# Performance work log

Hardware: AMD Instinct MI355X
Metric: run time of the kernel (lower is better)

The kernel has to match this reference:

```python
import jax, jax.numpy as jnp
import numpy as np

D_MODEL = 1024
NUM_HEADS = 16
D_K = D_MODEL // NUM_HEADS


def setup_inputs() -> dict:
    key = jax.random.key(0)
    ks = jax.random.split(key, 11)
    B, S, D = 2, 2048, D_MODEL
    scale = 1.0 / np.sqrt(D)
    inp = {
        'q': jax.random.normal(ks[0], (B, S, D), jnp.float32),
        'k': jax.random.normal(ks[1], (B, S, D), jnp.float32),
        'v': jax.random.normal(ks[2], (B, S, D), jnp.float32),
        'wq': jax.random.normal(ks[3], (D, D), jnp.float32) * scale,
        'bq': jnp.zeros((D,), jnp.float32),
        'wk': jax.random.normal(ks[4], (D, D), jnp.float32) * scale,
        'bk': jnp.zeros((D,), jnp.float32),
        'wv': jax.random.normal(ks[5], (D, D), jnp.float32) * scale,
        'bv': jnp.zeros((D,), jnp.float32),
        'wo': jax.random.normal(ks[6], (D, D), jnp.float32) * scale,
        'bo': jnp.zeros((D,), jnp.float32),
    }
    return inp


def _split_heads(x):
    B, S, _ = x.shape
    return x.reshape(B, S, NUM_HEADS, D_K).transpose(0, 2, 1, 3)  # [B,H,S,dk]


def reference(q, k, v, wq, bq, wk, bk, wv, bv, wo, bo):
    # Linear projections (torch Linear: x @ W^T + b)
    qh = _split_heads(q @ wq.T + bq)
    kh = _split_heads(k @ wk.T + bk)
    vh = _split_heads(v @ wv.T + bv)
    scores = jnp.einsum('bhqd,bhkd->bhqk', qh, kh) / np.sqrt(D_K)
    attn = jax.nn.softmax(scores, axis=-1)  # dropout is identity in eval
    ctx = jnp.einsum('bhqk,bhkd->bhqd', attn, vh)
    B, H, S, dk = ctx.shape
    ctx = ctx.transpose(0, 2, 1, 3).reshape(B, S, H * dk)
    return ctx @ wo.T + bo
```

## Files before the change

kernel.cpp:

```cpp
#include <hip/hip_runtime.h>
#include <hip/hip_bf16.h>
#include <math.h>

#define BATCH 2
#define SEQ   2048
#define DMODEL 1024
#define NHEAD 16
#define DK    64
#define M_TOT (BATCH*SEQ)
#define KDIM  DMODEL

typedef short bf16x8 __attribute__((ext_vector_type(8)));
typedef short bf16x4 __attribute__((ext_vector_type(4)));
typedef float f32x4  __attribute__((ext_vector_type(4)));
typedef __hip_bfloat16 bf16;

#define QSCALE 0.18033688011112042f

__device__ inline void gld_lds16(const void* g, void* l) {
    __builtin_amdgcn_global_load_lds(
        (const __attribute__((address_space(1))) unsigned int*)g,
        (__attribute__((address_space(3))) unsigned int*)l, 16, 0, 0);
}

__device__ inline unsigned pack2(float a, float b) {
    union { __hip_bfloat162 h; unsigned u; } t;
    t.h = __float22bfloat162_rn(make_float2(a, b));
    return t.u;
}

__global__ __launch_bounds__(256) void conv_all(
    const float* __restrict__ q, const float* __restrict__ k, const float* __restrict__ v,
    const float* __restrict__ wq, const float* __restrict__ wk,
    const float* __restrict__ wv, const float* __restrict__ wo,
    bf16* __restrict__ qh, bf16* __restrict__ kh, bf16* __restrict__ vh,
    bf16* __restrict__ wqh, bf16* __restrict__ wkh, bf16* __restrict__ wvh,
    bf16* __restrict__ woh)
{
    const int y = blockIdx.y;
    const int i = (blockIdx.x * 256 + threadIdx.x) * 4;
    if (y < 3) {
        const float* src = y == 0 ? q : (y == 1 ? k : v);
        bf16* dst = y == 0 ? qh : (y == 1 ? kh : vh);
        float4 t = *(const float4*)(src + i);
        uint2 o;
        o.x = pack2(t.x, t.y);
        o.y = pack2(t.z, t.w);
        *(uint2*)(dst + i) = o;
    } else {
        const int w = i >> 20;
        const int j = i & ((1 << 20) - 1);
        const float* src = w == 0 ? wq : (w == 1 ? wk : (w == 2 ? wv : wo));
        bf16* dsth = w == 0 ? wqh : (w == 1 ? wkh : (w == 2 ? wvh : woh));
        float4 t = *(const float4*)(src + j);
        uint2 oh;
        oh.x = pack2(t.x, t.y);
        oh.y = pack2(t.z, t.w);
        *(uint2*)(dsth + j) = oh;
    }
}

__device__ __forceinline__ void gemm_body(
    const bf16* __restrict__ Ah, const bf16* __restrict__ Wh,
    const float* __restrict__ bias, void* __restrict__ out,
    int layout, float scale, bf16* sA, bf16* sB, int kb, int ke,
    int row0, int col0)
{
    const int tid  = threadIdx.x;
    const int wave = tid >> 6, lane = tid & 63;
    const int ln   = lane & 15, quad = lane >> 4;
    const int wm   = wave >> 1, wn = wave & 1;

    const int srow = lane >> 2;
    const int clog = (lane & 3) ^ (srow & 3);
    const size_t gA0 = (size_t)(row0 + wave * 16 + srow) * KDIM + clog * 8;
    const size_t gB0 = (size_t)(col0 + wave * 16 + srow) * KDIM + clog * 8;
    const int ldsoff = (wave * 16 + srow) * 64 + (lane & 3) * 16;

    const int swz = (quad ^ (ln & 3)) * 8;

    f32x4 acc[4][4] = {};

    for (int k0 = kb; k0 < ke; k0 += 32) {
        __syncthreads();
#pragma unroll
        for (int j = 0; j < 2; ++j) {
            const size_t go = (size_t)k0 + (size_t)j * 64 * KDIM;
            gld_lds16(Ah + gA0 + go, (char*)sA + j * 4096 + ldsoff);
            gld_lds16(Wh + gB0 + go, (char*)sB + j * 4096 + ldsoff);
        }
        __syncthreads();

        bf16x8 af[4], bfr[4];
#pragma unroll
        for (int t = 0; t < 4; ++t) {
            af[t]  = *(const bf16x8*)&sA[(wm * 64 + t * 16 + ln) * 32 + swz];
            bfr[t] = *(const bf16x8*)&sB[(wn * 64 + t * 16 + ln) * 32 + swz];
        }
#pragma unroll
        for (int mt = 0; mt < 4; ++mt)
#pragma unroll
            for (int nt = 0; nt < 4; ++nt)
                acc[mt][nt] = __builtin_amdgcn_mfma_f32_16x16x32_bf16(af[mt], bfr[nt], acc[mt][nt], 0, 0, 0);
    }

#pragma unroll
    for (int nt = 0; nt < 4; ++nt) {
        const int n = col0 + wn * 64 + nt * 16 + ln;
        const float bv = (layout == 3) ? 0.f : bias[n];
#pragma unroll
        for (int mt = 0; mt < 4; ++mt) {
            const int m0 = row0 + wm * 64 + mt * 16 + quad * 4;
            if (layout == 0 || layout == 3) {
#pragma unroll
                for (int r = 0; r < 4; ++r)
                    ((float*)out)[(size_t)(m0 + r) * DMODEL + n] = (acc[mt][nt][r] + bv) * scale;
            } else if (layout == 1) {
                const int h = n >> 6, d = n & (DK - 1);
#pragma unroll
                for (int r = 0; r < 4; ++r) {
                    const int m = m0 + r;
                    const int b = m >> 11, s = m & (SEQ - 1);
                    ((bf16*)out)[((size_t)(b * NHEAD + h) * SEQ + s) * DK + d] =
                        __float2bfloat16((acc[mt][nt][r] + bv) * scale);
                }
            } else {
                const int h = n >> 6, d = n & (DK - 1);
                const int b = m0 >> 11, s0 = m0 & (SEQ - 1);
                union { bf16x4 v; uint2 u; } o4;
                o4.u.x = pack2((acc[mt][nt][0] + bv) * scale, (acc[mt][nt][1] + bv) * scale);
                o4.u.y = pack2((acc[mt][nt][2] + bv) * scale, (acc[mt][nt][3] + bv) * scale);
                *(bf16x4*)&((bf16*)out)[((size_t)(b * NHEAD + h) * DK + d) * SEQ + s0] = o4.v;
            }
        }
    }
}

struct QKVArgs {
    const bf16* A[3];
    const bf16* W[3];
    const float* bias[3];
    bf16* out[3];
    float scale[3];
    int layout[3];
};

__global__ __launch_bounds__(256) void qkv_gemm(QKVArgs a) {
    __shared__ __align__(16) bf16 sA[128 * 32];
    __shared__ __align__(16) bf16 sB[128 * 32];
    const int lin = (blockIdx.z * gridDim.y + blockIdx.y) * gridDim.x + blockIdx.x;
    const int xcd = lin & 7;
    const int r   = lin >> 3;
    const int z   = r >> 5;
    const int t   = r & 31;
    const int mt  = xcd * 4 + (t >> 3);
    const int nt  = t & 7;
    gemm_body(a.A[z], a.W[z], a.bias[z],
              (void*)a.out[z], a.layout[z], a.scale[z], sA, sB, 0, KDIM,
              mt * 128, nt * 128);
}

__global__ __launch_bounds__(256) void gemm_o(
    const bf16* __restrict__ Ah, const bf16* __restrict__ Wh,
    float* __restrict__ p0, float* __restrict__ p1)
{
    __shared__ __align__(16) bf16 sA[128 * 32];
    __shared__ __align__(16) bf16 sB[128 * 32];
    const int lin = (blockIdx.z * gridDim.y + blockIdx.y) * gridDim.x + blockIdx.x;
    const int xcd = lin & 7;
    const int r   = lin >> 3;
    const int z   = r >> 5;
    const int t   = r & 31;
    const int mt  = xcd * 4 + (t >> 3);
    const int nt  = t & 7;
    gemm_body(Ah, Wh, nullptr, (void*)(z ? p1 : p0), 3, 1.0f,
              sA, sB, z * (KDIM / 2), (z + 1) * (KDIM / 2),
              mt * 128, nt * 128);
}

__global__ __launch_bounds__(256) void combine_o(
    const float* __restrict__ p0, const float* __restrict__ p1,
    const float* __restrict__ bias, float* __restrict__ out)
{
    const int i = (blockIdx.x * 256 + threadIdx.x) * 4;
    float4 a = *(const float4*)(p0 + i);
    float4 b = *(const float4*)(p1 + i);
    float4 c = *(const float4*)(bias + (i & (DMODEL - 1)));
    float4 o;
    o.x = a.x + b.x + c.x;
    o.y = a.y + b.y + c.y;
    o.z = a.z + b.z + c.z;
    o.w = a.w + b.w + c.w;
    *(float4*)(out + i) = o;
}

#define NKT (SEQ / 64)
__global__ __launch_bounds__(256) void flash_attn_mfma(
    const bf16* __restrict__ Q, const bf16* __restrict__ K,
    const bf16* __restrict__ Vt, bf16* __restrict__ ctxh)
{
    __shared__ __align__(16) bf16 Vts[64 * 64];

    const int tid  = threadIdx.x;
    const int wave = tid >> 6, lane = tid & 63;
    const int ln   = lane & 15, quad = lane >> 4;

    const int lin  = blockIdx.y * gridDim.x + blockIdx.x;
    const int slot = lin >> 3;
    const int bh   = (lin & 7) * 4 + (slot >> 4);
    const int qt   = slot & 15;
    const int b    = bh >> 4, h = bh & (NHEAD - 1);

    const int q0 = qt * 128 + wave * 32;
    const bf16* Qb = Q + ((size_t)bh * SEQ + q0) * DK;
    bf16x8 qf[2][2];
#pragma unroll
    for (int c = 0; c < 2; ++c)
#pragma unroll
        for (int nt = 0; nt < 2; ++nt)
            qf[c][nt] = *(const bf16x8*)(Qb + (size_t)(nt * 16 + ln) * DK + c * 32 + quad * 8);

    f32x4 of[2][4] = {};
    float lp[2] = {0.f, 0.f};

    const int sr  = tid >> 2;
    const int scb = (tid & 3) * 2;
    const int ssw = sr & 7;
    const bf16* Vg0 = Vt + ((size_t)bh * DK + sr) * SEQ;
    const bf16* Kl  = K + (size_t)bh * SEQ * DK + (size_t)ln * DK + quad * 8;

    int vaddr[4];
#pragma unroll
    for (int mt = 0; mt < 4; ++mt)
        vaddr[mt] = ln * 64 + (((2 * mt + (quad >> 1)) ^ (ln & 7)) * 8) + (quad & 1) * 4;

    bf16x8 kfA[2][4], kfB[2][4];
#pragma unroll
    for (int c = 0; c < 2; ++c)
#pragma unroll
        for (int mt = 0; mt < 4; ++mt)
            kfA[c][mt] = *(const bf16x8*)(Kl + (size_t)(mt * 16) * DK + c * 32);

    auto halfiter = [&](int ktc, bf16x8 (&kfc)[2][4], bf16x8 (&kfn)[2][4]) {
        __syncthreads();
        {
            const bf16* Vg = Vg0 + ktc * 64;
            uint4 v0 = *(const uint4*)(Vg + scb * 8);
            uint4 v1 = *(const uint4*)(Vg + scb * 8 + 8);
            *(uint4*)(&Vts[sr * 64 + ((scb    ) ^ ssw) * 8]) = v0;
            *(uint4*)(&Vts[sr * 64 + ((scb + 1) ^ ssw) * 8]) = v1;
        }
        __syncthreads();

        const int ktn = (ktc + 1) & (NKT - 1);
#pragma unroll
        for (int c = 0; c < 2; ++c)
#pragma unroll
            for (int mt = 0; mt < 4; ++mt)
                kfn[c][mt] = *(const bf16x8*)(Kl + (size_t)(ktn * 64 + mt * 16) * DK + c * 32);

        f32x4 st[4][2] = {};
#pragma unroll
        for (int c = 0; c < 2; ++c)
#pragma unroll
            for (int mt = 0; mt < 4; ++mt)
#pragma unroll
                for (int nt = 0; nt < 2; ++nt)
                    st[mt][nt] = __builtin_amdgcn_mfma_f32_16x16x32_bf16(kfc[c][mt], qf[c][nt], st[mt][nt], 0, 0, 0);

        bf16x4 aP[4][2];
#pragma unroll
        for (int mt = 0; mt < 4; ++mt)
#pragma unroll
            for (int nt = 0; nt < 2; ++nt) {
                float p0 = __builtin_amdgcn_exp2f(st[mt][nt][0]);
                float p1 = __builtin_amdgcn_exp2f(st[mt][nt][1]);
                float p2 = __builtin_amdgcn_exp2f(st[mt][nt][2]);
                float p3 = __builtin_amdgcn_exp2f(st[mt][nt][3]);
                lp[nt] += (p0 + p1) + (p2 + p3);
                union { bf16x4 v; uint2 u; } uu;
                uu.u.x = pack2(p0, p1);
                uu.u.y = pack2(p2, p3);
                aP[mt][nt] = uu.v;
            }

#pragma unroll
        for (int mt = 0; mt < 4; ++mt)
#pragma unroll
            for (int nt = 0; nt < 4; ++nt) {
                bf16x4 vf = *(const bf16x4*)(&Vts[vaddr[mt] + nt * 1024]);
                of[0][nt] = __builtin_amdgcn_mfma_f32_16x16x16bf16_1k(aP[mt][0], vf, of[0][nt], 0, 0, 0);
                of[1][nt] = __builtin_amdgcn_mfma_f32_16x16x16bf16_1k(aP[mt][1], vf, of[1][nt], 0, 0, 0);
            }
    };

    for (int kt = 0; kt < NKT; kt += 2) {
        halfiter(kt,     kfA, kfB);
        halfiter(kt + 1, kfB, kfA);
    }

#pragma unroll
    for (int nt = 0; nt < 2; ++nt) {
        lp[nt] += __shfl_xor(lp[nt], 16, 64);
        lp[nt] += __shfl_xor(lp[nt], 32, 64);
    }
    float linv[2][4];
#pragma unroll
    for (int mtP = 0; mtP < 2; ++mtP)
#pragma unroll
        for (int r = 0; r < 4; ++r)
            linv[mtP][r] = 1.0f / __shfl(lp[mtP], quad * 4 + r, 64);

    const size_t base = ((size_t)b * SEQ + q0) * DMODEL + h * DK;
#pragma unroll
    for (int mtP = 0; mtP < 2; ++mtP)
#pragma unroll
        for (int nt = 0; nt < 4; ++nt)
#pragma unroll
            for (int r = 0; r < 4; ++r) {
                const float v = of[mtP][nt][r] * linv[mtP][r];
                const size_t idx = base + (size_t)(mtP * 16 + quad * 4 + r) * DMODEL + nt * 16 + ln;
                ctxh[idx] = __float2bfloat16(v);
            }
}

extern "C" void kernel_launch(void* const* d_in, const int* in_sizes, int n_in,
                              void* d_out, int out_size, void* d_ws, size_t ws_size,
                              hipStream_t stream) {
    const float* q  = (const float*)d_in[0];
    const float* k  = (const float*)d_in[1];
    const float* v  = (const float*)d_in[2];
    const float* wq = (const float*)d_in[3];
    const float* bq = (const float*)d_in[4];
    const float* wk = (const float*)d_in[5];
    const float* bk = (const float*)d_in[6];
    const float* wv = (const float*)d_in[7];
    const float* bv = (const float*)d_in[8];
    const float* wo = (const float*)d_in[9];
    const float* bo = (const float*)d_in[10];
    float* out = (float*)d_out;

    char* ws = (char*)d_ws;
    const size_t MB = 1u << 20;
    bf16* wq_hi = (bf16*)(ws + 0 * MB);
    bf16* wk_hi = (bf16*)(ws + 2 * MB);
    bf16* wv_hi = (bf16*)(ws + 4 * MB);
    bf16* wo_hi = (bf16*)(ws + 6 * MB);
    bf16* q_hi  = (bf16*)(ws + 8 * MB);
    bf16* k_hi  = (bf16*)(ws + 16 * MB);
    bf16* v_hi  = (bf16*)(ws + 24 * MB);
    bf16* Qp    = (bf16*)(ws + 32 * MB);
    bf16* Kp    = (bf16*)(ws + 40 * MB);
    bf16* Vpt   = (bf16*)(ws + 48 * MB);
    bf16* ctx_h = (bf16*)(ws + 8 * MB);
    float* p0   = (float*)(ws + 16 * MB);
    float* p1   = (float*)(ws + 32 * MB);

    const int NX = M_TOT * DMODEL;

    conv_all<<<dim3(NX / 1024, 4), 256, 0, stream>>>(
        q, k, v, wq, wk, wv, wo,
        q_hi, k_hi, v_hi, wq_hi, wk_hi, wv_hi, wo_hi);

    QKVArgs qa;
    qa.A[0] = q_hi;  qa.A[1] = k_hi;  qa.A[2] = v_hi;
    qa.W[0] = wq_hi; qa.W[1] = wk_hi; qa.W[2] = wv_hi;
    qa.bias[0] = bq; qa.bias[1] = bk; qa.bias[2] = bv;
    qa.out[0] = Qp;  qa.out[1] = Kp;  qa.out[2] = Vpt;
    qa.scale[0] = QSCALE; qa.scale[1] = 1.0f; qa.scale[2] = 1.0f;
    qa.layout[0] = 1; qa.layout[1] = 1; qa.layout[2] = 2;

    dim3 qgrid(DMODEL / 128, M_TOT / 128, 3);
    qkv_gemm<<<qgrid, 256, 0, stream>>>(qa);

    dim3 fgrid(SEQ / 128, BATCH * NHEAD);
    flash_attn_mfma<<<fgrid, 256, 0, stream>>>(Qp, Kp, Vpt, ctx_h);

    dim3 ogrid(DMODEL / 128, M_TOT / 128, 2);
    gemm_o<<<ogrid, 256, 0, stream>>>(ctx_h, wo_hi, p0, p1);

    combine_o<<<NX / 1024, 256, 0, stream>>>(p0, p1, bo, out);
}
```

Baseline: 264.6 us.

## Replace split-K output GEMM and combine with single 128x64-tile GEMM

The output projection previously ran as a split-K GEMM over two halves of K, writing two fp32 partials and then a separate combine kernel to sum them and add the bias. It now uses a dedicated kernel with 128x64 tiles over the full K, 512 blocks instead of 2x256, and adds the bias directly in the epilogue. This removes the extra fp32 partial writes and reads plus one launch. In exchange each block has a longer K loop and smaller N-tiles, so each A row-tile is loaded twice as often.

```diff
diff --git a/kernel.cpp b/kernel.cpp
--- a/kernel.cpp
+++ b/kernel.cpp
@@ -107,11 +107,11 @@
 #pragma unroll
     for (int nt = 0; nt < 4; ++nt) {
         const int n = col0 + wn * 64 + nt * 16 + ln;
-        const float bv = (layout == 3) ? 0.f : bias[n];
+        const float bv = bias ? bias[n] : 0.f;
 #pragma unroll
         for (int mt = 0; mt < 4; ++mt) {
             const int m0 = row0 + wm * 64 + mt * 16 + quad * 4;
-            if (layout == 0 || layout == 3) {
+            if (layout == 0) {
 #pragma unroll
                 for (int r = 0; r < 4; ++r)
                     ((float*)out)[(size_t)(m0 + r) * DMODEL + n] = (acc[mt][nt][r] + bv) * scale;
@@ -162,36 +162,70 @@
 
 __global__ __launch_bounds__(256) void gemm_o(
     const bf16* __restrict__ Ah, const bf16* __restrict__ Wh,
-    float* __restrict__ p0, float* __restrict__ p1)
+    const float* __restrict__ bias, float* __restrict__ out)
 {
     __shared__ __align__(16) bf16 sA[128 * 32];
-    __shared__ __align__(16) bf16 sB[128 * 32];
-    const int lin = (blockIdx.z * gridDim.y + blockIdx.y) * gridDim.x + blockIdx.x;
-    const int xcd = lin & 7;
-    const int r   = lin >> 3;
-    const int z   = r >> 5;
-    const int t   = r & 31;
-    const int mt  = xcd * 4 + (t >> 3);
-    const int nt  = t & 7;
-    gemm_body(Ah, Wh, nullptr, (void*)(z ? p1 : p0), 3, 1.0f,
-              sA, sB, z * (KDIM / 2), (z + 1) * (KDIM / 2),
-              mt * 128, nt * 128);
-}
-
-__global__ __launch_bounds__(256) void combine_o(
-    const float* __restrict__ p0, const float* __restrict__ p1,
-    const float* __restrict__ bias, float* __restrict__ out)
-{
-    const int i = (blockIdx.x * 256 + threadIdx.x) * 4;
-    float4 a = *(const float4*)(p0 + i);
-    float4 b = *(const float4*)(p1 + i);
-    float4 c = *(const float4*)(bias + (i & (DMODEL - 1)));
-    float4 o;
-    o.x = a.x + b.x + c.x;
-    o.y = a.y + b.y + c.y;
-    o.z = a.z + b.z + c.z;
-    o.w = a.w + b.w + c.w;
-    *(float4*)(out + i) = o;
+    __shared__ __align__(16) bf16 sB[64 * 32];
+
+    const int tid  = threadIdx.x;
+    const int wave = tid >> 6, lane = tid & 63;
+    const int ln   = lane & 15, quad = lane >> 4;
+    const int wm   = wave >> 1, wn = wave & 1;
+
+    const int lin  = blockIdx.y * gridDim.x + blockIdx.x;
+    const int xcd  = lin & 7;
+    const int r4   = lin >> 3;
+    const int row0 = (xcd * 4 + (r4 >> 4)) * 128;
+    const int col0 = (r4 & 15) * 64;
+
+    const int srow = lane >> 2;
+    const int clog = (lane & 3) ^ (srow & 3);
+    const size_t gA0 = (size_t)(row0 + wave * 16 + srow) * KDIM + clog * 8;
+    const int ldsoffA = (wave * 16 + srow) * 64 + (lane & 3) * 16;
+
+    const int brow  = tid >> 2;
+    const int bclog = (tid & 3) ^ (brow & 3);
+    const size_t gB0 = (size_t)(col0 + brow) * KDIM + bclog * 8;
+    const int ldsoffB = brow * 64 + (tid & 3) * 16;
+
+    const int swz = (quad ^ (ln & 3)) * 8;
+
+    f32x4 acc[4][2] = {};
+
+    for (int k0 = 0; k0 < KDIM; k0 += 32) {
+        __syncthreads();
+#pragma unroll
+        for (int j = 0; j < 2; ++j)
+            gld_lds16(Ah + gA0 + k0 + (size_t)j * 64 * KDIM, (char*)sA + j * 4096 + ldsoffA);
+        gld_lds16(Wh + gB0 + k0, (char*)sB + ldsoffB);
+        __syncthreads();
+
+        bf16x8 af[4], bfr[2];
+#pragma unroll
+        for (int t = 0; t < 4; ++t)
+            af[t] = *(const bf16x8*)&sA[(wm * 64 + t * 16 + ln) * 32 + swz];
+#pragma unroll
+        for (int t = 0; t < 2; ++t)
+            bfr[t] = *(const bf16x8*)&sB[(wn * 32 + t * 16 + ln) * 32 + swz];
+#pragma unroll
+        for (int mt = 0; mt < 4; ++mt)
+#pragma unroll
+            for (int nt = 0; nt < 2; ++nt)
+                acc[mt][nt] = __builtin_amdgcn_mfma_f32_16x16x32_bf16(af[mt], bfr[nt], acc[mt][nt], 0, 0, 0);
+    }
+
+#pragma unroll
+    for (int nt = 0; nt < 2; ++nt) {
+        const int n = col0 + wn * 32 + nt * 16 + ln;
+        const float bv = bias[n];
+#pragma unroll
+        for (int mt = 0; mt < 4; ++mt) {
+            const int m0 = row0 + wm * 64 + mt * 16 + quad * 4;
+#pragma unroll
+            for (int r = 0; r < 4; ++r)
+                out[(size_t)(m0 + r) * DMODEL + n] = acc[mt][nt][r] + bv;
+        }
+    }
 }
 
 #define NKT (SEQ / 64)
@@ -353,8 +387,6 @@
     bf16* Kp    = (bf16*)(ws + 40 * MB);
     bf16* Vpt   = (bf16*)(ws + 48 * MB);
     bf16* ctx_h = (bf16*)(ws + 8 * MB);
-    float* p0   = (float*)(ws + 16 * MB);
-    float* p1   = (float*)(ws + 32 * MB);
 
     const int NX = M_TOT * DMODEL;
 
@@ -376,8 +408,6 @@
     dim3 fgrid(SEQ / 128, BATCH * NHEAD);
     flash_attn_mfma<<<fgrid, 256, 0, stream>>>(Qp, Kp, Vpt, ctx_h);
 
-    dim3 ogrid(DMODEL / 128, M_TOT / 128, 2);
-    gemm_o<<<ogrid, 256, 0, stream>>>(ctx_h, wo_hi, p0, p1);
-
-    combine_o<<<NX / 1024, 256, 0, stream>>>(p0, p1, bo, out);
-}
+    dim3 ogrid(16, 32);
+    gemm_o<<<ogrid, 256, 0, stream>>>(ctx_h, wo_hi, bo, out);
+}
```

Result: faster. 256.5 us (median of 2 runs) (-3.0%).
